# Optimization experiments

Hardware: AMD Instinct MI355X
Metric: run time of the kernel (lower is better)

## Reference

```python
import jax, jax.numpy as jnp
import numpy as np

N_NODES = 100000
N_EDGES = 3200000
ALPHA = 0.9
N_LAYERS = 10


def setup_inputs() -> dict:
    key = jax.random.key(0)
    ks = jax.random.split(key, 6)
    x = jax.random.normal(ks[0], (N_NODES, 512), dtype=jnp.float32)
    W_in = jax.random.normal(ks[1], (256, 512), dtype=jnp.float32) * (1.0 / np.sqrt(512))
    b_in = jnp.zeros((256,), dtype=jnp.float32)
    W_out = jax.random.normal(ks[2], (64, 256), dtype=jnp.float32) * (1.0 / np.sqrt(256))
    b_out = jnp.zeros((64,), dtype=jnp.float32)
    edge_index = jax.random.randint(ks[3], (2, N_EDGES), 0, N_NODES, dtype=jnp.int64)
    # ~1/avg_degree scale keeps the iterated propagation numerically stable
    edge_weight = jax.random.uniform(ks[4], (N_EDGES,), dtype=jnp.float32) * (1.0 / 32.0)
    return {"x": x, "W_in": W_in, "b_in": b_in, "W_out": W_out,
            "b_out": b_out, "edge_index": edge_index, "edge_weight": edge_weight}


def _spmm(edge_index, edge_weight, z, n_nodes):
    # out[dst] += w * z[src]  (COO SpMM via gather + segment_sum)
    src, dst = edge_index[0], edge_index[1]
    msg = z[src] * edge_weight[:, None]            # [E, C]
    return jax.ops.segment_sum(msg, dst, num_segments=n_nodes)


def reference(x, W_in, b_in, W_out, b_out, edge_index, edge_weight):
    n_nodes = x.shape[0]
    h = jax.nn.relu(x @ W_in.T + b_in)             # linear_in -> (dropout: eval, identity) -> relu
    z = h @ W_out.T + b_out                        # linear_out: [N, n_classes]
    z0 = z
    for _ in range(N_LAYERS):
        # APPNP propagation: alpha-weighted adj propagation + residual blend with x_0
        z = ALPHA * _spmm(edge_index, edge_weight, z, n_nodes) + (1.0 - ALPHA) * z0
    return z
```

## Files before the change

### kernel.cpp

```cpp
#include <hip/hip_runtime.h>
#include <hip/hip_bf16.h>

typedef __attribute__((ext_vector_type(8))) short bf16x8;
typedef __attribute__((ext_vector_type(4))) float f32x4;

__device__ __forceinline__ short f2b(float f) {
    unsigned u = __builtin_bit_cast(unsigned, f);
    unsigned r = (u + 0x7fffu + ((u >> 16) & 1u)) >> 16;
    return (short)r;
}
__device__ __forceinline__ unsigned f2bu(float f) {
    unsigned u = __builtin_bit_cast(unsigned, f);
    return ((u + 0x7fffu + ((u >> 16) & 1u)) >> 16) & 0xffffu;
}
__device__ __forceinline__ float blo(unsigned u) {
    return __builtin_bit_cast(float, u << 16);
}
__device__ __forceinline__ float bhi(unsigned u) {
    return __builtin_bit_cast(float, u & 0xffff0000u);
}

__global__ __launch_bounds__(256) void wprep(
    const float* __restrict__ W_in, const float* __restrict__ W_out,
    unsigned short* __restrict__ Wi_f, unsigned short* __restrict__ Wo_f)
{
    int o = blockIdx.x * 256 + threadIdx.x;
    if (o < 131072) {
        int j = o & 7, lane = (o >> 3) & 63, t = (o >> 9) & 15, kk = o >> 13;
        int n = t * 16 + (lane & 15);
        int k = kk * 32 + ((lane >> 4) << 3) + j;
        Wi_f[o] = (unsigned short)f2bu(W_in[n * 512 + k]);
    } else if (o < 131072 + 16384) {
        int o2 = o - 131072;
        int j = o2 & 7, lane = (o2 >> 3) & 63, t = (o2 >> 9) & 3, kk2 = o2 >> 11;
        int n = t * 16 + (lane & 15);
        int k = kk2 * 32 + ((lane >> 4) << 3) + j;
        Wo_f[o2] = (unsigned short)f2bu(W_out[n * 256 + k]);
    }
}

__global__ __launch_bounds__(256) void mlp(
    const float* __restrict__ x, const unsigned short* __restrict__ Wi_f,
    const float* __restrict__ b_in, const unsigned short* __restrict__ Wo_f,
    const float* __restrict__ b_out, unsigned short* __restrict__ z0, int M)
{
    __shared__ __align__(16) char smem[33280];
    short* Bt0 = (short*)smem;
    short* Bt1 = (short*)(smem + 16384);
    short* Hs  = (short*)smem;

    const int tid  = threadIdx.x;
    const int lane = tid & 63;
    const int w    = tid >> 6;
    const int row0 = blockIdx.x * 64;
    const int c    = lane & 15;
    const int qk   = lane >> 4;

    const int growA = row0 + 16 * w + c;
    const float* xrow = x + (size_t)(growA < M ? growA : (M - 1)) * 512 + qk * 8;

    f32x4 acc[16];
#pragma unroll
    for (int t = 0; t < 16; ++t) { acc[t][0]=0.f; acc[t][1]=0.f; acc[t][2]=0.f; acc[t][3]=0.f; }

    float4 av0 = *(const float4*)(xrow);
    float4 av1 = *(const float4*)(xrow + 4);
#pragma unroll
    for (int i = 0; i < 4; ++i) {
        int t = w * 4 + i;
        const unsigned short* g = Wi_f + ((size_t)t * 64 + lane) * 8;
        __builtin_amdgcn_global_load_lds(
            (const __attribute__((address_space(1))) unsigned int*)g,
            (__attribute__((address_space(3))) unsigned int*)(Bt0 + t * 512),
            16, 0, 0);
    }
    __syncthreads();

    for (int kk = 0; kk < 16; ++kk) {
        short* Bc = (kk & 1) ? Bt1 : Bt0;
        short* Bn = (kk & 1) ? Bt0 : Bt1;
        float4 a0 = av0, a1 = av1;
        if (kk < 15) {
            const float* xn = xrow + (kk + 1) * 32;
            av0 = *(const float4*)(xn);
            av1 = *(const float4*)(xn + 4);
#pragma unroll
            for (int i = 0; i < 4; ++i) {
                int t = w * 4 + i;
                const unsigned short* g = Wi_f + (((size_t)(kk + 1) * 16 + t) * 64 + lane) * 8;
                __builtin_amdgcn_global_load_lds(
                    (const __attribute__((address_space(1))) unsigned int*)g,
                    (__attribute__((address_space(3))) unsigned int*)(Bn + t * 512),
                    16, 0, 0);
            }
        }
        bf16x8 a;
        a[0] = (short)f2bu(a0.x); a[1] = (short)f2bu(a0.y);
        a[2] = (short)f2bu(a0.z); a[3] = (short)f2bu(a0.w);
        a[4] = (short)f2bu(a1.x); a[5] = (short)f2bu(a1.y);
        a[6] = (short)f2bu(a1.z); a[7] = (short)f2bu(a1.w);
#pragma unroll
        for (int t = 0; t < 16; ++t) {
            bf16x8 b = *(const bf16x8*)(Bc + (t * 64 + lane) * 8);
            acc[t] = __builtin_amdgcn_mfma_f32_16x16x32_bf16(a, b, acc[t], 0, 0, 0);
        }
        __syncthreads();
    }

#pragma unroll
    for (int t = 0; t < 16; ++t) {
        int col = 16 * t + c;
        float bv = b_in[col];
        int qb = col >> 3, j = col & 7;
#pragma unroll
        for (int r = 0; r < 4; ++r) {
            int row = 16 * w + qk * 4 + r;
            float h = acc[t][r] + bv;
            h = h > 0.f ? h : 0.f;
            Hs[qb * 520 + row * 8 + j] = f2b(h);
        }
    }
    __syncthreads();
    f32x4 acc2[4];
#pragma unroll
    for (int t = 0; t < 4; ++t) { acc2[t][0]=0.f; acc2[t][1]=0.f; acc2[t][2]=0.f; acc2[t][3]=0.f; }
#pragma unroll
    for (int kk2 = 0; kk2 < 8; ++kk2) {
        bf16x8 a2 = *(const bf16x8*)(Hs + (kk2 * 4 + qk) * 520 + (16 * w + c) * 8);
#pragma unroll
        for (int t = 0; t < 4; ++t) {
            bf16x8 b2 = *(const bf16x8*)(Wo_f + (((size_t)kk2 * 4 + t) * 64 + lane) * 8);
            acc2[t] = __builtin_amdgcn_mfma_f32_16x16x32_bf16(a2, b2, acc2[t], 0, 0, 0);
        }
    }
#pragma unroll
    for (int t = 0; t < 4; ++t) {
        int col = 16 * t + c;
        float bv = b_out[col];
#pragma unroll
        for (int r = 0; r < 4; ++r) {
            int grow = row0 + 16 * w + qk * 4 + r;
            if (grow < M) z0[(size_t)grow * 64 + col] = (unsigned short)f2bu(acc2[t][r] + bv);
        }
    }
}

#define CSR_CH   16384
#define MAXBUK   256

__global__ __launch_bounds__(256) void coarse_hist(
    const int* __restrict__ dst, int* __restrict__ M, int E, int nbuk)
{
    __shared__ int cnt[MAXBUK];
    int tid = threadIdx.x, blk = blockIdx.x;
    for (int i = tid; i < nbuk; i += 256) cnt[i] = 0;
    __syncthreads();
    int e0 = blk * CSR_CH, e1 = e0 + CSR_CH; if (e1 > E) e1 = E;
    for (int e = e0 + tid; e < e1; e += 256) atomicAdd(&cnt[dst[e] >> 9], 1);
    __syncthreads();
    for (int i = tid; i < nbuk; i += 256) M[blk * nbuk + i] = cnt[i];
}

__global__ __launch_bounds__(256) void bucket_scan(
    int* __restrict__ M, int* __restrict__ bucketBase, int nblk, int nbuk)
{
    __shared__ int tot[MAXBUK];
    int tid = threadIdx.x;
    for (int r = tid; r < nbuk; r += 256) {
        int s = 0;
        for (int k = 0; k < nblk; ++k) s += M[k * nbuk + r];
        tot[r] = s;
    }
    __syncthreads();
    if (tid == 0) {
        int s = 0;
        for (int r = 0; r < nbuk; ++r) { int t = tot[r]; tot[r] = s; bucketBase[r] = s; s += t; }
        bucketBase[nbuk] = s;
    }
    __syncthreads();
    for (int r = tid; r < nbuk; r += 256) {
        int s = tot[r];
        for (int k = 0; k < nblk; ++k) { int t = M[k * nbuk + r]; M[k * nbuk + r] = s; s += t; }
    }
}

__global__ __launch_bounds__(256) void coarse_scatter(
    const int* __restrict__ src, const int* __restrict__ dst,
    const float* __restrict__ ew, const int* __restrict__ M,
    int4* __restrict__ tmp, int E, int nbuk)
{
    __shared__ int off[MAXBUK];
    int tid = threadIdx.x, blk = blockIdx.x;
    for (int i = tid; i < nbuk; i += 256) off[i] = M[blk * nbuk + i];
    __syncthreads();
    int e0 = blk * CSR_CH, e1 = e0 + CSR_CH; if (e1 > E) e1 = E;
    for (int e = e0 + tid; e < e1; e += 256) {
        int d = dst[e];
        int pos = atomicAdd(&off[d >> 9], 1);
        tmp[pos] = make_int4(src[e], __builtin_bit_cast(int, ew[e]), d, 0);
    }
}

__global__ __launch_bounds__(256) void fine_sort(
    const int4* __restrict__ tmp, const int* __restrict__ bucketBase,
    int2* __restrict__ csr, int* __restrict__ rowptr, int N, int E)
{
    __shared__ int fc[512];
    __shared__ int fo[512];
    __shared__ int wsum[5];
    int b = blockIdx.x, tid = threadIdx.x;
    int base = bucketBase[b], cnt = bucketBase[b + 1] - base;
    int node0 = b << 9;

    fc[tid] = 0; fc[tid + 256] = 0;
    __syncthreads();
    for (int i = tid; i < cnt; i += 256)
        atomicAdd(&fc[tmp[base + i].z - node0], 1);
    __syncthreads();

    int lane = tid & 63, wid = tid >> 6;
    int runbase = 0;
    for (int h = 0; h < 2; ++h) {
        int v = fc[h * 256 + tid];
        int x = v;
#pragma unroll
        for (int off = 1; off < 64; off <<= 1) { int y = __shfl_up(x, off); if (lane >= off) x += y; }
        if (lane == 63) wsum[wid] = x;
        __syncthreads();
        if (tid == 0) { int s = 0; for (int k = 0; k < 4; ++k) { int t = wsum[k]; wsum[k] = s; s += t; } wsum[4] = s; }
        __syncthreads();
        fo[h * 256 + tid] = runbase + wsum[wid] + x - v;
        runbase += wsum[4];
        __syncthreads();
    }

    for (int i = tid; i < 512; i += 256) {
        int node = node0 + i;
        if (node < N) rowptr[node] = base + fo[i];
    }
    if (b == 0 && tid == 0) rowptr[N] = E;
    __syncthreads();

    for (int i = tid; i < cnt; i += 256) {
        int4 ed = tmp[base + i];
        int pos = atomicAdd(&fo[ed.z - node0], 1);
        csr[base + pos] = make_int2(ed.x, ed.y);
    }
}

__global__ __launch_bounds__(256) void prop_kernel(
    const int* __restrict__ rowptr, const int2* __restrict__ csr,
    const unsigned short* __restrict__ zin, const unsigned short* __restrict__ z0,
    unsigned short* __restrict__ zout_b, float* __restrict__ zout_f,
    int n, int final_layer)
{
    int lane = threadIdx.x & 63;
    int node = blockIdx.x * 4 + (threadIdx.x >> 6);
    if (node >= n) return;
    int beg = rowptr[node], end = rowptr[node + 1];
    const int sub = lane >> 3;
    const int k8  = lane & 7;

    float acc[8];
#pragma unroll
    for (int i = 0; i < 8; ++i) acc[i] = 0.f;

    for (int b = beg; b < end; b += 64) {
        int e = b + lane;
        long long edp = (e < end)
            ? __builtin_nontemporal_load((const long long*)csr + e)
            : 0ll;
        int edx = (int)(edp & 0xffffffffll);
        int edy = (int)(edp >> 32);
        int cnt = end - b; if (cnt > 64) cnt = 64;
        int nq = (cnt + 31) >> 5;
        for (int g = 0; g < nq; ++g) {
            int sj[4]; float wj[4];
#pragma unroll
            for (int q = 0; q < 4; ++q) {
                int idx = g * 32 + q * 8 + sub;
                sj[q] = __shfl(edx, idx);
                int wb = __shfl(edy, idx);
                wj[q] = (idx < cnt) ? __builtin_bit_cast(float, wb) : 0.f;
            }
            uint4 v[4];
#pragma unroll
            for (int q = 0; q < 4; ++q)
                v[q] = *(const uint4*)(zin + (size_t)sj[q] * 64 + k8 * 8);
#pragma unroll
            for (int q = 0; q < 4; ++q) {
                float w_ = wj[q];
                acc[0] += w_ * blo(v[q].x); acc[1] += w_ * bhi(v[q].x);
                acc[2] += w_ * blo(v[q].y); acc[3] += w_ * bhi(v[q].y);
                acc[4] += w_ * blo(v[q].z); acc[5] += w_ * bhi(v[q].z);
                acc[6] += w_ * blo(v[q].w); acc[7] += w_ * bhi(v[q].w);
            }
        }
    }
#pragma unroll
    for (int off = 8; off < 64; off <<= 1) {
#pragma unroll
        for (int i = 0; i < 8; ++i) acc[i] += __shfl_xor(acc[i], off);
    }
    if (sub == 0) {
        uint4 zv = *(const uint4*)(z0 + (size_t)node * 64 + k8 * 8);
        float o0 = 0.9f * acc[0] + 0.1f * blo(zv.x);
        float o1 = 0.9f * acc[1] + 0.1f * bhi(zv.x);
        float o2 = 0.9f * acc[2] + 0.1f * blo(zv.y);
        float o3 = 0.9f * acc[3] + 0.1f * bhi(zv.y);
        float o4 = 0.9f * acc[4] + 0.1f * blo(zv.z);
        float o5 = 0.9f * acc[5] + 0.1f * bhi(zv.z);
        float o6 = 0.9f * acc[6] + 0.1f * blo(zv.w);
        float o7 = 0.9f * acc[7] + 0.1f * bhi(zv.w);
        if (final_layer) {
            float* dp = zout_f + (size_t)node * 64 + k8 * 8;
            *(float4*)dp       = make_float4(o0, o1, o2, o3);
            *(float4*)(dp + 4) = make_float4(o4, o5, o6, o7);
        } else {
            uint4 pv;
            pv.x = f2bu(o0) | (f2bu(o1) << 16);
            pv.y = f2bu(o2) | (f2bu(o3) << 16);
            pv.z = f2bu(o4) | (f2bu(o5) << 16);
            pv.w = f2bu(o6) | (f2bu(o7) << 16);
            *(uint4*)(zout_b + (size_t)node * 64 + k8 * 8) = pv;
        }
    }
}

static inline size_t align_up(size_t v, size_t a) { return (v + a - 1) & ~(a - 1); }

extern "C" void kernel_launch(void* const* d_in, const int* in_sizes, int n_in,
                              void* d_out, int out_size, void* d_ws, size_t ws_size,
                              hipStream_t stream)
{
    const float* x     = (const float*)d_in[0];
    const float* W_in  = (const float*)d_in[1];
    const float* b_in  = (const float*)d_in[2];
    const float* W_out = (const float*)d_in[3];
    const float* b_out = (const float*)d_in[4];
    const int*   ei    = (const int*)d_in[5];
    const float* ew    = (const float*)d_in[6];

    const int N = in_sizes[0] / 512;
    const int E = in_sizes[6];
    const int* e_src = ei;
    const int* e_dst = ei + E;

    const int nbuk = (N + 511) >> 9;
    const int nblk = (E + CSR_CH - 1) / CSR_CH;

    char* p = (char*)d_ws;
    size_t zbytes = align_up((size_t)N * 64 * sizeof(unsigned short), 256);
    unsigned short* z0b = (unsigned short*)p; p += zbytes;
    unsigned short* Wi_f = (unsigned short*)p; p += align_up(131072 * 2, 256);
    unsigned short* Wo_f = (unsigned short*)p; p += align_up(16384 * 2, 256);
    int2* csr   = (int2*)p; p += align_up((size_t)E * 8, 256);
    int* rowptr = (int*)p;  p += align_up((size_t)(N + 1) * 4, 256);
    int* M      = (int*)p;  p += align_up((size_t)nblk * nbuk * 4, 256);
    int* bucketBase = (int*)p; p += align_up((size_t)(nbuk + 1) * 4, 256);
    int4* tmp   = (int4*)p; p += align_up((size_t)E * 16, 256);
    unsigned short* zA = (unsigned short*)tmp;
    unsigned short* zB = zA + (size_t)N * 64;

    wprep<<<(131072 + 16384 + 255) / 256, 256, 0, stream>>>(W_in, W_out, Wi_f, Wo_f);
    mlp<<<(N + 63) / 64, 256, 0, stream>>>(x, Wi_f, b_in, Wo_f, b_out, z0b, N);

    coarse_hist<<<nblk, 256, 0, stream>>>(e_dst, M, E, nbuk);
    bucket_scan<<<1, 256, 0, stream>>>(M, bucketBase, nblk, nbuk);
    coarse_scatter<<<nblk, 256, 0, stream>>>(e_src, e_dst, ew, M, tmp, E, nbuk);
    fine_sort<<<nbuk, 256, 0, stream>>>(tmp, bucketBase, csr, rowptr, N, E);

    float* out_f = (float*)d_out;
    int pgrid = (N + 3) / 4;
    for (int i = 0; i < 10; ++i) {
        const unsigned short* zin = (i == 0) ? z0b : ((i & 1) ? zA : zB);
        unsigned short* zoutb = (i & 1) ? zB : zA;
        prop_kernel<<<pgrid, 256, 0, stream>>>(rowptr, csr, zin, z0b,
                                               zoutb, out_f, N, (i == 9) ? 1 : 0);
    }
}
```

Baseline: 1.213 ms.

## Store propagation features in column-chunk layout and split nodes across four chunk blocks

The bf16 z arrays are re-laid out as four column-chunks of 16 features each, so every node row in a chunk is 32 contiguous bytes. The MLP output writes directly into this layout. The propagation grid becomes four times larger, with each block handling one chunk for four nodes and two lanes covering each edge's 16 features. The aim is a smaller per-chunk gather working set and more edges in flight per wave. In exchange, each node's CSR segment is read four times, and each random gather is only 32 bytes, which can waste cache-line bandwidth. The z0 loads and intermediate stores also switch to nontemporal hints.

```diff
diff --git a/kernel.cpp b/kernel.cpp
--- a/kernel.cpp
+++ b/kernel.cpp
@@ -3,6 +3,7 @@
 
 typedef __attribute__((ext_vector_type(8))) short bf16x8;
 typedef __attribute__((ext_vector_type(4))) float f32x4;
+typedef __attribute__((ext_vector_type(4))) unsigned int u32x4;
 
 __device__ __forceinline__ short f2b(float f) {
     unsigned u = __builtin_bit_cast(unsigned, f);
@@ -137,10 +138,11 @@
     for (int t = 0; t < 4; ++t) {
         int col = 16 * t + c;
         float bv = b_out[col];
+        size_t cbase = (size_t)(col >> 4) * M * 16 + (col & 15);
 #pragma unroll
         for (int r = 0; r < 4; ++r) {
             int grow = row0 + 16 * w + qk * 4 + r;
-            if (grow < M) z0[(size_t)grow * 64 + col] = (unsigned short)f2bu(acc2[t][r] + bv);
+            if (grow < M) z0[cbase + (size_t)grow * 16] = (unsigned short)f2bu(acc2[t][r] + bv);
         }
     }
 }
@@ -254,56 +256,53 @@
     unsigned short* __restrict__ zout_b, float* __restrict__ zout_f,
     int n, int final_layer)
 {
-    int lane = threadIdx.x & 63;
-    int node = blockIdx.x * 4 + (threadIdx.x >> 6);
+    const int b     = blockIdx.x;
+    const int chunk = b & 3;
+    const int nblk  = b >> 2;
+    const int node  = nblk * 4 + (threadIdx.x >> 6);
     if (node >= n) return;
+    const int lane = threadIdx.x & 63;
+    const int sub  = lane >> 1;
+    const int k2   = lane & 1;
+    const size_t coff = (size_t)chunk * n * 16;
+    const unsigned short* zc = zin + coff;
+
     int beg = rowptr[node], end = rowptr[node + 1];
-    const int sub = lane >> 3;
-    const int k8  = lane & 7;
 
     float acc[8];
 #pragma unroll
     for (int i = 0; i < 8; ++i) acc[i] = 0.f;
 
-    for (int b = beg; b < end; b += 64) {
-        int e = b + lane;
+    for (int bb = beg; bb < end; bb += 64) {
+        int e = bb + lane;
         long long edp = (e < end)
             ? __builtin_nontemporal_load((const long long*)csr + e)
             : 0ll;
         int edx = (int)(edp & 0xffffffffll);
         int edy = (int)(edp >> 32);
-        int cnt = end - b; if (cnt > 64) cnt = 64;
-        int nq = (cnt + 31) >> 5;
-        for (int g = 0; g < nq; ++g) {
-            int sj[4]; float wj[4];
-#pragma unroll
-            for (int q = 0; q < 4; ++q) {
-                int idx = g * 32 + q * 8 + sub;
-                sj[q] = __shfl(edx, idx);
-                int wb = __shfl(edy, idx);
-                wj[q] = (idx < cnt) ? __builtin_bit_cast(float, wb) : 0.f;
-            }
-            uint4 v[4];
-#pragma unroll
-            for (int q = 0; q < 4; ++q)
-                v[q] = *(const uint4*)(zin + (size_t)sj[q] * 64 + k8 * 8);
-#pragma unroll
-            for (int q = 0; q < 4; ++q) {
-                float w_ = wj[q];
-                acc[0] += w_ * blo(v[q].x); acc[1] += w_ * bhi(v[q].x);
-                acc[2] += w_ * blo(v[q].y); acc[3] += w_ * bhi(v[q].y);
-                acc[4] += w_ * blo(v[q].z); acc[5] += w_ * bhi(v[q].z);
-                acc[6] += w_ * blo(v[q].w); acc[7] += w_ * bhi(v[q].w);
-            }
-        }
-    }
-#pragma unroll
-    for (int off = 8; off < 64; off <<= 1) {
+        int cnt = end - bb; if (cnt > 64) cnt = 64;
+        int ng = (cnt + 31) >> 5;
+        for (int g = 0; g < ng; ++g) {
+            int idx = g * 32 + sub;
+            int sj = __shfl(edx, idx);
+            int wb = __shfl(edy, idx);
+            float wj = (idx < cnt) ? __builtin_bit_cast(float, wb) : 0.f;
+            u32x4 v = *(const u32x4*)(zc + (size_t)sj * 16 + k2 * 8);
+            acc[0] += wj * blo(v.x); acc[1] += wj * bhi(v.x);
+            acc[2] += wj * blo(v.y); acc[3] += wj * bhi(v.y);
+            acc[4] += wj * blo(v.z); acc[5] += wj * bhi(v.z);
+            acc[6] += wj * blo(v.w); acc[7] += wj * bhi(v.w);
+        }
+    }
+#pragma unroll
+    for (int off = 2; off < 64; off <<= 1) {
 #pragma unroll
         for (int i = 0; i < 8; ++i) acc[i] += __shfl_xor(acc[i], off);
     }
     if (sub == 0) {
-        uint4 zv = *(const uint4*)(z0 + (size_t)node * 64 + k8 * 8);
+        const unsigned short* z0c = z0 + coff;
+        u32x4 zv = __builtin_nontemporal_load(
+            (const u32x4*)(z0c + (size_t)node * 16 + k2 * 8));
         float o0 = 0.9f * acc[0] + 0.1f * blo(zv.x);
         float o1 = 0.9f * acc[1] + 0.1f * bhi(zv.x);
         float o2 = 0.9f * acc[2] + 0.1f * blo(zv.y);
@@ -313,16 +312,17 @@
         float o6 = 0.9f * acc[6] + 0.1f * blo(zv.w);
         float o7 = 0.9f * acc[7] + 0.1f * bhi(zv.w);
         if (final_layer) {
-            float* dp = zout_f + (size_t)node * 64 + k8 * 8;
+            float* dp = zout_f + (size_t)node * 64 + chunk * 16 + k2 * 8;
             *(float4*)dp       = make_float4(o0, o1, o2, o3);
             *(float4*)(dp + 4) = make_float4(o4, o5, o6, o7);
         } else {
-            uint4 pv;
+            u32x4 pv;
             pv.x = f2bu(o0) | (f2bu(o1) << 16);
             pv.y = f2bu(o2) | (f2bu(o3) << 16);
             pv.z = f2bu(o4) | (f2bu(o5) << 16);
             pv.w = f2bu(o6) | (f2bu(o7) << 16);
-            *(uint4*)(zout_b + (size_t)node * 64 + k8 * 8) = pv;
+            __builtin_nontemporal_store(
+                pv, (u32x4*)(zout_b + coff + (size_t)node * 16 + k2 * 8));
         }
     }
 }
@@ -371,7 +371,8 @@
     fine_sort<<<nbuk, 256, 0, stream>>>(tmp, bucketBase, csr, rowptr, N, E);
 
     float* out_f = (float*)d_out;
-    int pgrid = (N + 3) / 4;
+    int NB = (N + 3) / 4;
+    int pgrid = NB * 4;
     for (int i = 0; i < 10; ++i) {
         const unsigned short* zin = (i == 0) ? z0b : ((i & 1) ? zA : zB);
         unsigned short* zoutb = (i & 1) ? zB : zA;
```

Measured after the change: 2.440 ms. +101.1%, slower.
